# Optimization experiments

Hardware: AMD Instinct MI355X
Metric: run time of the kernel (lower is better)

The kernel has to match this reference:

```python
import jax, jax.numpy as jnp
import numpy as np

REFSIZE = 1024  # init kwarg refsize -> self.N
EPS = float(np.finfo(np.float32).eps)


def interp1d(x, y, xnew):
    """Batched linear interpolation, faithful to Interp1d.forward.
    x, y: (D, N) with x sorted along last dim; xnew: (D, P). Returns (D, P)."""
    # torch.searchsorted default (right=False) == numpy/jnp side='left'
    ind = jax.vmap(jnp.searchsorted)(x, xnew) - 1
    ind = jnp.clip(ind, 0, x.shape[1] - 2)
    slopes = (y[:, 1:] - y[:, :-1]) / (EPS + (x[:, 1:] - x[:, :-1]))
    x_sel = jnp.take_along_axis(x, ind, axis=1)
    y_sel = jnp.take_along_axis(y, ind, axis=1)
    s_sel = jnp.take_along_axis(slopes, ind, axis=1)
    return y_sel + s_sel * (xnew - x_sel)


def setup_inputs() -> dict:
    key = jax.random.key(0)
    k1, k2 = jax.random.split(key)
    l, n = 2048, 4096
    x1 = jax.random.uniform(k1, (l, n), dtype=jnp.float32)  # points on [0,1)
    w = jax.random.uniform(k2, (l, n), dtype=jnp.float32)
    x1_weights = w / jnp.sum(w, axis=-1, keepdims=True)  # row-normalized masses
    return {"x1": x1, "x1_weights": x1_weights}


def reference(x1, x1_weights):
    l, n = x1.shape
    N = REFSIZE
    ref = jnp.linspace(0.0, 1.0, N + 1, dtype=jnp.float32)[:-1]  # (N,)

    # empirical_cdf: sort samples, cumsum weights
    order = jnp.argsort(x1, axis=-1)
    xs = jnp.take_along_axis(x1, order, axis=-1)          # (l, n) sorted samples
    ys = jnp.cumsum(jnp.take_along_axis(x1_weights, order, axis=-1), axis=-1)  # CDF

    # emb
    alpha = (jnp.sum(x1 * x1_weights, axis=-1) / jnp.sum(x1_weights, axis=-1) - 0.5)[:, None]
    xnew = jnp.broadcast_to(jnp.linspace(-1.0, 2.0, 3 * N, dtype=jnp.float32)[None, :], (l, 3 * N))
    int_x = jnp.floor(xnew)
    rest_x = xnew - int_x
    ecdf = int_x + interp1d(xs, ys, rest_x)               # (l, 3N) extended CDF

    x_grid = jnp.broadcast_to(ref[None, :], (l, N))
    embedd = interp1d(ecdf, xnew, x_grid - alpha) - x_grid  # inverse-CDF embedding

    # circular cost
    a = jnp.abs(embedd)
    m = jnp.minimum(a, 1.0 - a)
    return jnp.sqrt(jnp.mean(jnp.sum(m * m, axis=-1)) + 1e-8)
```

## Files before the change

### kernel.cpp

```cpp
#include <hip/hip_runtime.h>
#include <math.h>

#define L    2048
#define NCOL 4096
#define NG   1024
#define N3   3072
#define T    512
#define NW   8
#define EPT  8
#define NB   2048
#define BPT  (NB / T)
#define FEPS 1.1920929e-07f

typedef unsigned long long u64;

__device__ __forceinline__ int lower_bound_f(const float* a, int lo, int hi, float v) {
  while (lo < hi) {
    int mid = (lo + hi) >> 1;
    if (a[mid] < v) lo = mid + 1; else hi = mid;
  }
  return lo;
}

__device__ __forceinline__ int bucket_of(u64 k) {
  float f = __uint_as_float((unsigned)(k >> 32));
  int b = (int)(f * (float)NB);
  return b > NB - 1 ? NB - 1 : b;
}

__global__ __launch_bounds__(T, 2) void lcot_rows(const float* __restrict__ X,
                                                  const float* __restrict__ W,
                                                  float* __restrict__ rowsum) {
  extern __shared__ char smem[];
  u64*   pairs = (u64*)smem;
  float* xs    = (float*)smem;
  float* ys    = xs + NCOL;
  int*   cnt   = (int*)(smem + 32768);
  float* ecdf  = (float*)(smem + 32768 + 8208);
  unsigned short* lut2 = (unsigned short*)(smem + 32768 + 8208 + 12288);

  __shared__ float redA[NW], redB[NW], fwt[NW];
  __shared__ int   iwt[NW];
  __shared__ float s_alpha;

  const int tid  = threadIdx.x;
  const int lane = tid & 63;
  const int wave = tid >> 6;
  const int row  = blockIdx.x;
  const float* xr = X + (size_t)row * NCOL;
  const float* wr = W + (size_t)row * NCOL;

#pragma unroll
  for (int i = 0; i < BPT; ++i) cnt[tid + i * T] = 0;

  u64 key[EPT]; float wv[EPT];
  float sxw = 0.f, sw = 0.f;
  const float4* xr4 = (const float4*)xr;
  const float4* wr4 = (const float4*)wr;
#pragma unroll
  for (int c = 0; c < 2; ++c) {
    float4 xv = xr4[tid * 2 + c];
    float4 ww = wr4[tid * 2 + c];
    sxw += xv.x * ww.x + xv.y * ww.y + xv.z * ww.z + xv.w * ww.w;
    sw  += ww.x + ww.y + ww.z + ww.w;
    int b = 8 * tid + 4 * c;
    key[4*c+0] = ((u64)__float_as_uint(xv.x) << 32) | (unsigned)(b + 0);
    key[4*c+1] = ((u64)__float_as_uint(xv.y) << 32) | (unsigned)(b + 1);
    key[4*c+2] = ((u64)__float_as_uint(xv.z) << 32) | (unsigned)(b + 2);
    key[4*c+3] = ((u64)__float_as_uint(xv.w) << 32) | (unsigned)(b + 3);
    wv[4*c+0] = ww.x; wv[4*c+1] = ww.y; wv[4*c+2] = ww.z; wv[4*c+3] = ww.w;
  }
#pragma unroll
  for (int off = 32; off > 0; off >>= 1) {
    sxw += __shfl_down(sxw, off);
    sw  += __shfl_down(sw, off);
  }
  if (lane == 0) { redA[wave] = sxw; redB[wave] = sw; }
  __syncthreads();

  int ord[EPT];
#pragma unroll
  for (int e = 0; e < EPT; ++e) ord[e] = atomicAdd(&cnt[bucket_of(key[e])], 1);
  __syncthreads();
  if (tid == 0) {
    float a = 0.f, b = 0.f;
#pragma unroll
    for (int i = 0; i < NW; ++i) { a += redA[i]; b += redB[i]; }
    s_alpha = a / b - 0.5f;
  }

  int c4[BPT];
  int runi = 0;
#pragma unroll
  for (int j = 0; j < BPT; ++j) { c4[j] = cnt[tid * BPT + j]; runi += c4[j]; }
  int toti = runi, prei = runi;
#pragma unroll
  for (int off = 1; off < 64; off <<= 1) {
    int v = __shfl_up(prei, off);
    if (lane >= off) prei += v;
  }
  if (lane == 63) iwt[wave] = prei;
  __syncthreads();
  int wpre = 0;
#pragma unroll
  for (int w2 = 0; w2 < NW; ++w2) wpre += (w2 < wave) ? iwt[w2] : 0;
  int acc = wpre + prei - toti;
#pragma unroll
  for (int j = 0; j < BPT; ++j) { int t2 = acc; acc += c4[j]; cnt[tid * BPT + j] = t2; }
  if (tid == T - 1) cnt[NB] = acc;
  __syncthreads();

#pragma unroll
  for (int e = 0; e < EPT; ++e) pairs[cnt[bucket_of(key[e])] + ord[e]] = key[e];
  __syncthreads();

  int p[EPT];
#pragma unroll
  for (int e = 0; e < EPT; ++e) {
    int b = bucket_of(key[e]);
    int lo = cnt[b], m = cnt[b + 1] - lo;
    int r = 0;
    for (int q = 0; q < m; ++q) r += (pairs[lo + q] < key[e]) ? 1 : 0;
    p[e] = lo + r;
  }
  __syncthreads();

#pragma unroll
  for (int e = 0; e < EPT; ++e) {
    xs[p[e]] = __uint_as_float((unsigned)(key[e] >> 32));
    ys[p[e]] = wv[e];
  }
  __syncthreads();

  float lw[EPT];
  {
    const float4* y4 = (const float4*)(ys + EPT * tid);
    float4 a0 = y4[0], a1 = y4[1];
    lw[0]=a0.x; lw[1]=a0.y; lw[2]=a0.z; lw[3]=a0.w;
    lw[4]=a1.x; lw[5]=a1.y; lw[6]=a1.z; lw[7]=a1.w;
  }
  float runf = 0.f;
#pragma unroll
  for (int c = 0; c < EPT; ++c) { runf += lw[c]; lw[c] = runf; }
  float totf = runf, pref = runf;
#pragma unroll
  for (int off = 1; off < 64; off <<= 1) {
    float v = __shfl_up(pref, off);
    if (lane >= off) pref += v;
  }
  if (lane == 63) fwt[wave] = pref;
  __syncthreads();
  float wpf = 0.f;
#pragma unroll
  for (int w2 = 0; w2 < NW; ++w2) wpf += (w2 < wave) ? fwt[w2] : 0.f;
  float basef = wpf + pref - totf;
  {
    float4* y4 = (float4*)(ys + EPT * tid);
    y4[0] = make_float4(basef+lw[0], basef+lw[1], basef+lw[2], basef+lw[3]);
    y4[1] = make_float4(basef+lw[4], basef+lw[5], basef+lw[6], basef+lw[7]);
  }
  __syncthreads();

#pragma unroll
  for (int s = 0; s < N3 / T; ++s) {
    int j = tid + s * T;
    float xnew = -1.0f + (3.0f * (float)j) / 3071.0f;
    float ix = floorf(xnew);
    float rest = xnew - ix;
    int k = (int)(rest * (float)NB);
    k = k > NB - 1 ? NB - 1 : k;
    int lo = lower_bound_f(xs, cnt[k], cnt[k + 1], rest);
    int ind = lo - 1;
    ind = ind < 0 ? 0 : (ind > NCOL - 2 ? NCOL - 2 : ind);
    float x0 = xs[ind], x1v = xs[ind + 1];
    float y0 = ys[ind], y1v = ys[ind + 1];
    float slope = (y1v - y0) / (FEPS + (x1v - x0));
    ecdf[j] = ix + (y0 + slope * (rest - x0));
  }
  __syncthreads();

  if (tid < 257) {
    float v = -1.0f + 3.0f * (float)tid * (1.0f / 256.0f);
    lut2[tid] = (unsigned short)lower_bound_f(ecdf, 0, N3, v);
  }
  __syncthreads();

  float alpha = s_alpha;
  float accf = 0.f;
#pragma unroll
  for (int s = 0; s < NG / T; ++s) {
    int kq = tid + s * T;
    float xg = (float)kq / 1024.0f;
    float q = xg - alpha;
    int k2 = (int)floorf((q + 1.0f) * (256.0f / 3.0f));
    k2 = k2 < 0 ? 0 : (k2 > 255 ? 255 : k2);
    int blo = k2 > 0 ? k2 - 1 : 0;
    int bhi = k2 < 254 ? k2 + 2 : 256;
    int lo = lower_bound_f(ecdf, lut2[blo], lut2[bhi], q);
    int ind = lo - 1;
    ind = ind < 0 ? 0 : (ind > N3 - 2 ? N3 - 2 : ind);
    float e0 = ecdf[ind], e1 = ecdf[ind + 1];
    float y0 = -1.0f + (3.0f * (float)ind) / 3071.0f;
    float y1 = -1.0f + (3.0f * (float)(ind + 1)) / 3071.0f;
    float slope = (y1 - y0) / (FEPS + (e1 - e0));
    float emb = y0 + slope * (q - e0) - xg;
    float a = fabsf(emb);
    float m = fminf(a, 1.0f - a);
    accf += m * m;
  }
#pragma unroll
  for (int off = 32; off > 0; off >>= 1) accf += __shfl_down(accf, off);
  if (lane == 0) redA[wave] = accf;
  __syncthreads();
  if (tid == 0) {
    float s = 0.f;
#pragma unroll
    for (int i = 0; i < NW; ++i) s += redA[i];
    rowsum[row] = s;
  }
}

__global__ __launch_bounds__(256) void lcot_final(const float* __restrict__ rowsum,
                                                  float* __restrict__ out) {
  __shared__ float red[4];
  int t = threadIdx.x;
  float s = 0.f;
  for (int i = t; i < L; i += 256) s += rowsum[i];
#pragma unroll
  for (int off = 32; off > 0; off >>= 1) s += __shfl_down(s, off);
  if ((t & 63) == 0) red[t >> 6] = s;
  __syncthreads();
  if (t == 0) {
    float tot = red[0] + red[1] + red[2] + red[3];
    out[0] = sqrtf(tot / (float)L + 1e-8f);
  }
}

extern "C" void kernel_launch(void* const* d_in, const int* in_sizes, int n_in,
                              void* d_out, int out_size, void* d_ws, size_t ws_size,
                              hipStream_t stream) {
  const float* X = (const float*)d_in[0];
  const float* W = (const float*)d_in[1];
  float* rowsum = (float*)d_ws;
  size_t shbytes = 32768 + 8208 + 12288 + 520;
  hipLaunchKernelGGL(lcot_rows, dim3(L), dim3(T), shbytes, stream, X, W, rowsum);
  hipLaunchKernelGGL(lcot_final, dim3(1), dim3(256), 0, stream,
                     (const float*)rowsum, (float*)d_out);
}
```

Before: 189.7 us.

## Shrink shared memory with 16-bit packed counters and aliased ecdf buffer

Bucket counters become 16-bit values packed two per 32-bit word, so atomics add 65536 or 1 depending on bucket parity. The ecdf buffer now aliases the ys region, with values held in registers across an added barrier before they are written. Dynamic LDS per block drops from about 53KB to about 37KB and launch bounds ask for more blocks per CU, aiming for higher occupancy. The cost is extra barriers, pack/unpack arithmetic, and possible register pressure from the stricter launch bound.

```diff
diff --git a/kernel.cpp b/kernel.cpp
--- a/kernel.cpp
+++ b/kernel.cpp
@@ -9,10 +9,11 @@
 #define NW   8
 #define EPT  8
 #define NB   2048
-#define BPT  (NB / T)
 #define FEPS 1.1920929e-07f
 
 typedef unsigned long long u64;
+typedef unsigned short u16;
+typedef unsigned int u32;
 
 __device__ __forceinline__ int lower_bound_f(const float* a, int lo, int hi, float v) {
   while (lo < hi) {
@@ -22,22 +23,23 @@
   return lo;
 }
 
-__device__ __forceinline__ int bucket_of(u64 k) {
-  float f = __uint_as_float((unsigned)(k >> 32));
+__device__ __forceinline__ int bucket_of_bits(unsigned xb) {
+  float f = __uint_as_float(xb);
   int b = (int)(f * (float)NB);
   return b > NB - 1 ? NB - 1 : b;
 }
 
-__global__ __launch_bounds__(T, 2) void lcot_rows(const float* __restrict__ X,
+__global__ __launch_bounds__(T, 8) void lcot_rows(const float* __restrict__ X,
                                                   const float* __restrict__ W,
                                                   float* __restrict__ rowsum) {
   extern __shared__ char smem[];
   u64*   pairs = (u64*)smem;
   float* xs    = (float*)smem;
-  float* ys    = xs + NCOL;
-  int*   cnt   = (int*)(smem + 32768);
-  float* ecdf  = (float*)(smem + 32768 + 8208);
-  unsigned short* lut2 = (unsigned short*)(smem + 32768 + 8208 + 12288);
+  float* ys    = (float*)(smem + 16384);
+  float* ecdf  = (float*)(smem + 16384);
+  u16*   cnt16 = (u16*)(smem + 32768);
+  u32*   cntw  = (u32*)(smem + 32768);
+  u16*   lut2  = (u16*)(smem + 36872);
 
   __shared__ float redA[NW], redB[NW], fwt[NW];
   __shared__ int   iwt[NW];
@@ -50,8 +52,7 @@
   const float* xr = X + (size_t)row * NCOL;
   const float* wr = W + (size_t)row * NCOL;
 
-#pragma unroll
-  for (int i = 0; i < BPT; ++i) cnt[tid + i * T] = 0;
+  for (int i = tid; i < 1025; i += T) cntw[i] = 0u;
 
   u64 key[EPT]; float wv[EPT];
   float sxw = 0.f, sw = 0.f;
@@ -80,7 +81,12 @@
 
   int ord[EPT];
 #pragma unroll
-  for (int e = 0; e < EPT; ++e) ord[e] = atomicAdd(&cnt[bucket_of(key[e])], 1);
+  for (int e = 0; e < EPT; ++e) {
+    int b = bucket_of_bits((unsigned)(key[e] >> 32));
+    u32 inc = (b & 1) ? 65536u : 1u;
+    u32 ret = atomicAdd(&cntw[b >> 1], inc);
+    ord[e] = (b & 1) ? (int)(ret >> 16) : (int)(ret & 0xffffu);
+  }
   __syncthreads();
   if (tid == 0) {
     float a = 0.f, b = 0.f;
@@ -89,10 +95,10 @@
     s_alpha = a / b - 0.5f;
   }
 
-  int c4[BPT];
-  int runi = 0;
-#pragma unroll
-  for (int j = 0; j < BPT; ++j) { c4[j] = cnt[tid * BPT + j]; runi += c4[j]; }
+  u32 cv0 = cntw[2 * tid], cv1 = cntw[2 * tid + 1];
+  int c0 = (int)(cv0 & 0xffffu), c1 = (int)(cv0 >> 16);
+  int c2 = (int)(cv1 & 0xffffu), c3 = (int)(cv1 >> 16);
+  int runi = c0 + c1 + c2 + c3;
   int toti = runi, prei = runi;
 #pragma unroll
   for (int off = 1; off < 64; off <<= 1) {
@@ -105,20 +111,29 @@
 #pragma unroll
   for (int w2 = 0; w2 < NW; ++w2) wpre += (w2 < wave) ? iwt[w2] : 0;
   int acc = wpre + prei - toti;
-#pragma unroll
-  for (int j = 0; j < BPT; ++j) { int t2 = acc; acc += c4[j]; cnt[tid * BPT + j] = t2; }
-  if (tid == T - 1) cnt[NB] = acc;
-  __syncthreads();
-
-#pragma unroll
-  for (int e = 0; e < EPT; ++e) pairs[cnt[bucket_of(key[e])] + ord[e]] = key[e];
+  {
+    int b0 = acc; acc += c0;
+    int b1 = acc; acc += c1;
+    int b2 = acc; acc += c2;
+    int b3 = acc; acc += c3;
+    cntw[2 * tid]     = (u32)b0 | ((u32)b1 << 16);
+    cntw[2 * tid + 1] = (u32)b2 | ((u32)b3 << 16);
+  }
+  if (tid == T - 1) cnt16[NB] = (u16)acc;
+  __syncthreads();
+
+#pragma unroll
+  for (int e = 0; e < EPT; ++e) {
+    int b = bucket_of_bits((unsigned)(key[e] >> 32));
+    pairs[(int)cnt16[b] + ord[e]] = key[e];
+  }
   __syncthreads();
 
   int p[EPT];
 #pragma unroll
   for (int e = 0; e < EPT; ++e) {
-    int b = bucket_of(key[e]);
-    int lo = cnt[b], m = cnt[b + 1] - lo;
+    int b = bucket_of_bits((unsigned)(key[e] >> 32));
+    int lo = (int)cnt16[b], m = (int)cnt16[b + 1] - lo;
     int r = 0;
     for (int q = 0; q < m; ++q) r += (pairs[lo + q] < key[e]) ? 1 : 0;
     p[e] = lo + r;
@@ -161,6 +176,7 @@
   }
   __syncthreads();
 
+  float ev[N3 / T];
 #pragma unroll
   for (int s = 0; s < N3 / T; ++s) {
     int j = tid + s * T;
@@ -169,19 +185,23 @@
     float rest = xnew - ix;
     int k = (int)(rest * (float)NB);
     k = k > NB - 1 ? NB - 1 : k;
-    int lo = lower_bound_f(xs, cnt[k], cnt[k + 1], rest);
+    int lo = lower_bound_f(xs, (int)cnt16[k], (int)cnt16[k + 1], rest);
     int ind = lo - 1;
     ind = ind < 0 ? 0 : (ind > NCOL - 2 ? NCOL - 2 : ind);
     float x0 = xs[ind], x1v = xs[ind + 1];
     float y0 = ys[ind], y1v = ys[ind + 1];
     float slope = (y1v - y0) / (FEPS + (x1v - x0));
-    ecdf[j] = ix + (y0 + slope * (rest - x0));
-  }
+    ev[s] = ix + (y0 + slope * (rest - x0));
+  }
+  __syncthreads();
+
+#pragma unroll
+  for (int s = 0; s < N3 / T; ++s) ecdf[tid + s * T] = ev[s];
   __syncthreads();
 
   if (tid < 257) {
     float v = -1.0f + 3.0f * (float)tid * (1.0f / 256.0f);
-    lut2[tid] = (unsigned short)lower_bound_f(ecdf, 0, N3, v);
+    lut2[tid] = (u16)lower_bound_f(ecdf, 0, N3, v);
   }
   __syncthreads();
 
@@ -196,7 +216,7 @@
     k2 = k2 < 0 ? 0 : (k2 > 255 ? 255 : k2);
     int blo = k2 > 0 ? k2 - 1 : 0;
     int bhi = k2 < 254 ? k2 + 2 : 256;
-    int lo = lower_bound_f(ecdf, lut2[blo], lut2[bhi], q);
+    int lo = lower_bound_f(ecdf, (int)lut2[blo], (int)lut2[bhi], q);
     int ind = lo - 1;
     ind = ind < 0 ? 0 : (ind > N3 - 2 ? N3 - 2 : ind);
     float e0 = ecdf[ind], e1 = ecdf[ind + 1];
@@ -242,7 +262,7 @@
   const float* X = (const float*)d_in[0];
   const float* W = (const float*)d_in[1];
   float* rowsum = (float*)d_ws;
-  size_t shbytes = 32768 + 8208 + 12288 + 520;
+  size_t shbytes = 32768 + 4104 + 520;
   hipLaunchKernelGGL(lcot_rows, dim3(L), dim3(T), shbytes, stream, X, W, rowsum);
   hipLaunchKernelGGL(lcot_final, dim3(1), dim3(256), 0, stream,
                      (const float*)rowsum, (float*)d_out);
```

After: 181.8 us. 1.04x faster.
